# Kernel optimization log

Hardware: AMD Instinct MI355X
Metric: run time of the kernel (lower is better)

## Reference

```python
import jax, jax.numpy as jnp
import numpy as np

SLOPE = 25.0   # snntorch surrogate.fast_sigmoid default slope
THR = 1.0      # snntorch Leaky default threshold
BETA = 0.95
SPIKE_STEPS = 4
NUM_HEADS = 16

@jax.custom_vjp
def spike(u):
    # Heaviside forward, fast-sigmoid surrogate backward
    return (u > 0).astype(u.dtype)

def _spike_fwd(u):
    return spike(u), u

def _spike_bwd(u, g):
    return (g / (SLOPE * jnp.abs(u) + 1.0) ** 2,)

spike.defvjp(_spike_fwd, _spike_bwd)

def lif_mean(cur):
    """Run SPIKE_STEPS of a snntorch Leaky neuron (subtract reset, detached)
    with constant input current `cur`; return mean spike train over time."""
    def step(mem, _):
        reset = jax.lax.stop_gradient(spike(mem - THR))
        mem = BETA * mem + cur - reset * THR
        return mem, spike(mem - THR)
    _, spk = jax.lax.scan(step, jnp.zeros_like(cur), None, length=SPIKE_STEPS)
    return spk.mean(axis=0)

def setup_inputs() -> dict:
    B, S, D = 2, 2048, 1024
    key = jax.random.key(0)
    ks = jax.random.split(key, 9)
    std = 1.0 / np.sqrt(D)
    mkw = lambda k: jax.random.uniform(k, (D, D), jnp.float32, -std, std)
    mkb = lambda k: jax.random.uniform(k, (D,), jnp.float32, -std, std)
    return {
        "x": jax.random.normal(ks[0], (B, S, D), jnp.float32),
        "q_w": mkw(ks[1]), "q_b": mkb(ks[2]),
        "k_w": mkw(ks[3]), "k_b": mkb(ks[4]),
        "v_w": mkw(ks[5]), "v_b": mkb(ks[6]),
        "o_w": mkw(ks[7]), "o_b": mkb(ks[8]),
    }

def reference(x, q_w, q_b, k_w, k_b, v_w, v_b, o_w, o_b):
    B, S, D = x.shape
    H = NUM_HEADS
    Hd = D // H
    # projections -> [B, H, S, Hd]  (weights stored [in, out])
    proj = lambda w, b: (x @ w + b).reshape(B, S, H, Hd).transpose(0, 2, 1, 3)
    q, k, v = proj(q_w, q_b), proj(k_w, k_b), proj(v_w, v_b)
    # LIF spiking recurrence, aggregated over time
    q_agg, k_agg, v_agg = lif_mean(q), lif_mean(k), lif_mean(v)
    # standard scaled dot-product attention on aggregated spikes
    scores = jnp.einsum('bhqd,bhkd->bhqk', q_agg, k_agg) / jnp.sqrt(jnp.float32(Hd))
    attn = jax.nn.softmax(scores, axis=-1)
    out = jnp.einsum('bhqk,bhkd->bhqd', attn, v_agg)
    out = out.transpose(0, 2, 1, 3).reshape(B, S, D)
    return out @ o_w + o_b
```

## Files before the change

kernel.cpp:

```cpp
#include <hip/hip_runtime.h>
#include <hip/hip_bf16.h>
#include <stdint.h>

typedef unsigned short u16;
typedef unsigned int u32;
typedef __bf16 bf16x8 __attribute__((ext_vector_type(8)));
typedef float f32x4 __attribute__((ext_vector_type(4)));
typedef float f32x16 __attribute__((ext_vector_type(16)));
typedef u32 u32x4 __attribute__((ext_vector_type(4)));

#define B_   2
#define S_   2048
#define D_   1024
#define H_   16
#define HD_  64

__device__ __forceinline__ u16 f2bf(float f) {
    u32 u = __float_as_uint(f);
    u32 r = (u + 0x7FFFu + ((u >> 16) & 1u)) >> 16;
    return (u16)r;
}
__device__ __forceinline__ float bf2f(u16 s) { return __uint_as_float(((u32)s) << 16); }

__device__ __forceinline__ f32x4 mfma16(bf16x8 a, bf16x8 b, f32x4 c) {
    return __builtin_amdgcn_mfma_f32_16x16x32_bf16(a, b, c, 0, 0, 0);
}
__device__ __forceinline__ f32x16 mfma32(bf16x8 a, bf16x8 b, f32x16 c) {
    return __builtin_amdgcn_mfma_f32_32x32x16_bf16(a, b, c, 0, 0, 0);
}

__device__ __forceinline__ void gl16(const u16* g, u16* l) {
    __builtin_amdgcn_global_load_lds(
        (const __attribute__((address_space(1))) void*)g,
        (__attribute__((address_space(3))) void*)l, 16, 0, 0);
}

__global__ void prep_kernel(const float* __restrict__ x,
                            const float* __restrict__ qw, const float* __restrict__ kw,
                            const float* __restrict__ vw, const float* __restrict__ ow,
                            u16* __restrict__ xbf, u16* __restrict__ wt_all) {
    __shared__ float tile[32][33];
    const int bid = blockIdx.x;
    const int t = threadIdx.x;
    if (bid < 4096) {
        int i = bid * 256 + t;
        float4 v = reinterpret_cast<const float4*>(x)[i];
        uint2 hp;
        hp.x = (u32)f2bf(v.x) | ((u32)f2bf(v.y) << 16);
        hp.y = (u32)f2bf(v.z) | ((u32)f2bf(v.w) << 16);
        reinterpret_cast<uint2*>(xbf)[i] = hp;
        return;
    }
    const int f = bid - 4096;
    const int z = f >> 10;
    const int bi = (f & 1023) >> 5;
    const int bj = f & 31;
    const float* w = (z == 0) ? qw : (z == 1) ? kw : (z == 2) ? vw : ow;
    u16* thi = wt_all + (size_t)z * 1048576;
    const int tx = t & 31, ty = t >> 5;
#pragma unroll
    for (int k = 0; k < 4; k++) {
        int r = ty + k * 8;
        tile[r][tx] = w[(size_t)(bi * 32 + r) * D_ + bj * 32 + tx];
    }
    __syncthreads();
#pragma unroll
    for (int k = 0; k < 4; k++) {
        int r = ty + k * 8;
        thi[(size_t)(bj * 32 + r) * D_ + bi * 32 + tx] = f2bf(tile[tx][r]);
    }
}

__global__ __launch_bounds__(256, 3)
void qkv_gemm(const u16* __restrict__ Ag, const u16* __restrict__ Bg,
              const float* __restrict__ qb, const float* __restrict__ kb,
              const float* __restrict__ vb,
              u16* __restrict__ o0, u16* __restrict__ o1, u16* __restrict__ o2) {
    __shared__ __align__(16) u16 lA[3][128 * 32];
    __shared__ __align__(16) u16 lB[3][128 * 32];

    const int t = threadIdx.x;
    const int flat = blockIdx.y * 24 + blockIdx.x;
    const int swz = (flat & 7) * 96 + (flat >> 3);
    const int m0 = (swz / 24) * 128;
    const int n0 = (swz % 24) * 128;
    const int wid = t >> 6, lane = t & 63;
    const int wm = wid >> 1, wn = wid & 1;
    const int lr = lane & 15, lg = lane >> 4;

    f32x4 acc[4][4] = {};

    auto STAGE = [&](int buf, int kk) {
        const int k0 = kk * 32;
#pragma unroll
        for (int p = 0; p < 2; p++) {
            int idx = p * 256 + wid * 64 + lane;
            int row = idx >> 2, sl = idx & 3;
            int slx = sl ^ ((row >> 1) & 3);
            gl16(Ag + (size_t)(m0 + row) * D_ + k0 + slx * 8,
                 &lA[buf][(p * 256 + wid * 64) * 8]);
            gl16(Bg + (size_t)(n0 + row) * D_ + k0 + slx * 8,
                 &lB[buf][(p * 256 + wid * 64) * 8]);
        }
    };

    STAGE(0, 0);
    STAGE(1, 1);

    for (int kk = 0; kk < 32; ++kk) {
        if (kk < 31) asm volatile("s_waitcnt vmcnt(4)" ::: "memory");
        else         asm volatile("s_waitcnt vmcnt(0)" ::: "memory");
        __builtin_amdgcn_s_barrier();
        if (kk < 30) STAGE((kk + 2) % 3, kk + 2);

        const int cur = kk % 3;
        bf16x8 af[4], bf[4];
#pragma unroll
        for (int m = 0; m < 4; m++) {
            int row = wm * 64 + m * 16 + lr;
            af[m] = *reinterpret_cast<const bf16x8*>(
                &lA[cur][row * 32 + (lg ^ ((row >> 1) & 3)) * 8]);
        }
#pragma unroll
        for (int n = 0; n < 4; n++) {
            int row = wn * 64 + n * 16 + lr;
            bf[n] = *reinterpret_cast<const bf16x8*>(
                &lB[cur][row * 32 + (lg ^ ((row >> 1) & 3)) * 8]);
        }
#pragma unroll
        for (int m = 0; m < 4; m++)
#pragma unroll
            for (int n = 0; n < 4; n++)
                acc[m][n] = mfma16(af[m], bf[n], acc[m][n]);
    }

    const int col0f = n0 + wn * 64;
    const int proj = col0f >> 10;
    const float* bp = (proj == 0) ? qb : (proj == 1) ? kb : vb;
    u16* dst = (proj == 0) ? o0 : (proj == 1) ? o1 : o2;
#pragma unroll
    for (int m = 0; m < 4; m++) {
#pragma unroll
        for (int n = 0; n < 4; n++) {
            u16 agg4[4];
#pragma unroll
            for (int r = 0; r < 4; r++) {
                int row = m0 + wm * 64 + m * 16 + lg * 4 + r;
                int colp = (col0f + n * 16 + lr) & 1023;
                float cur_i = acc[m][n][r] + bp[colp];
                float mem = 0.f;
                int cnt = 0;
#pragma unroll
                for (int tt = 0; tt < 4; tt++) {
                    float reset = (mem > 1.f) ? 1.f : 0.f;
                    mem = 0.95f * mem;
                    mem = mem + cur_i;
                    mem = mem - reset;
                    cnt += (mem > 1.f) ? 1 : 0;
                }
                u16 agg = (u16)(__float_as_uint((float)cnt * 0.25f) >> 16);
                if (proj != 2) {
                    int b = row >> 11, s = row & 2047;
                    int h = colp >> 6, d = colp & 63;
                    dst[((size_t)(b * H_ + h) * S_ + s) * HD_ + d] = agg;
                } else {
                    agg4[r] = agg;
                }
            }
            if (proj == 2) {
                int row0 = m0 + wm * 64 + m * 16 + lg * 4;
                int colp = (col0f + n * 16 + lr) & 1023;
                int b = row0 >> 11, s = row0 & 2047;
                int h = colp >> 6, d = colp & 63;
                uint2 pk;
                pk.x = (u32)agg4[0] | ((u32)agg4[1] << 16);
                pk.y = (u32)agg4[2] | ((u32)agg4[3] << 16);
                *reinterpret_cast<uint2*>(
                    &dst[((size_t)(b * H_ + h) * HD_ + d) * S_ + s]) = pk;
            }
        }
    }
}

__global__ __launch_bounds__(256, 4)
void o_gemm(const u16* __restrict__ Ag, const u16* __restrict__ Bhg,
            const float* __restrict__ bias, float* __restrict__ out) {
    __shared__ __align__(16) u16 lA[3][64 * 32];
    __shared__ __align__(16) u16 lB[3][64 * 32];

    const int t = threadIdx.x;
    const int flat = blockIdx.y * 16 + blockIdx.x;
    const int swz = (flat & 7) * 128 + (flat >> 3);
    const int m0 = (swz >> 4) * 64;
    const int n0 = (swz & 15) * 64;
    const int wid = t >> 6, lane = t & 63;
    const int wm = wid >> 1, wn = wid & 1;
    const int lr = lane & 15, lg = lane >> 4;

    f32x4 acc[2][2] = {};

    auto STAGE = [&](int buf, int kk) {
        const int k0 = kk * 32;
        int idx = wid * 64 + lane;
        int row = idx >> 2, sl = idx & 3;
        int slx = sl ^ ((row >> 1) & 3);
        gl16(Ag + (size_t)(m0 + row) * D_ + k0 + slx * 8,
             &lA[buf][(wid * 64) * 8]);
        gl16(Bhg + (size_t)(n0 + row) * D_ + k0 + slx * 8,
             &lB[buf][(wid * 64) * 8]);
    };

    STAGE(0, 0);
    STAGE(1, 1);

    for (int kk = 0; kk < 32; ++kk) {
        if (kk < 31) asm volatile("s_waitcnt vmcnt(2)" ::: "memory");
        else         asm volatile("s_waitcnt vmcnt(0)" ::: "memory");
        __builtin_amdgcn_s_barrier();
        if (kk < 30) STAGE((kk + 2) % 3, kk + 2);

        const int cur = kk % 3;
        bf16x8 af[2], bf[2];
#pragma unroll
        for (int m = 0; m < 2; m++) {
            int row = wm * 32 + m * 16 + lr;
            af[m] = *reinterpret_cast<const bf16x8*>(
                &lA[cur][row * 32 + (lg ^ ((row >> 1) & 3)) * 8]);
        }
#pragma unroll
        for (int n = 0; n < 2; n++) {
            int row = wn * 32 + n * 16 + lr;
            bf[n] = *reinterpret_cast<const bf16x8*>(
                &lB[cur][row * 32 + (lg ^ ((row >> 1) & 3)) * 8]);
        }
#pragma unroll
        for (int m = 0; m < 2; m++)
#pragma unroll
            for (int n = 0; n < 2; n++)
                acc[m][n] = mfma16(af[m], bf[n], acc[m][n]);
    }

#pragma unroll
    for (int m = 0; m < 2; m++)
#pragma unroll
        for (int n = 0; n < 2; n++)
#pragma unroll
            for (int r = 0; r < 4; r++) {
                int row = m0 + wm * 32 + m * 16 + lg * 4 + r;
                int col = n0 + wn * 32 + n * 16 + lr;
                out[(size_t)row * D_ + col] = acc[m][n][r] + bias[col];
            }
}

__global__ __launch_bounds__(512, 1)
void attn_kernel(const u16* __restrict__ qa, const u16* __restrict__ ka,
                 const u16* __restrict__ vt, u16* __restrict__ oag) {
    __shared__ __align__(16) u16 Kb[3][2][64 * 64];
    __shared__ __align__(16) u16 Vb[3][2][64 * 64];

    const int t = threadIdx.x;
    const int wid = t >> 6, lane = t & 63;
    const int l31 = lane & 31, hi = lane >> 5;
    const int sx = l31 & 7;

    const int flat = blockIdx.y * 8 + blockIdx.x;
    const int swz = (flat & 7) * 32 + (flat >> 3);
    const int bh = swz >> 3;
    const int q0 = (swz & 7) * 256;

    const u16* qbase = qa + (size_t)bh * S_ * HD_;
    const u16* kbase = ka + (size_t)bh * S_ * HD_;
    const u16* vbase = vt + (size_t)bh * HD_ * S_;

    bf16x8 qf[4];
#pragma unroll
    for (int kc = 0; kc < 4; kc++)
        qf[kc] = *reinterpret_cast<const bf16x8*>(
            qbase + (size_t)(q0 + wid * 32 + l31) * HD_ + kc * 16 + hi * 8);

    bf16x8 ones;
#pragma unroll
    for (int j = 0; j < 8; j++) ones[j] = (__bf16)1.0f;

    f32x16 oacc0 = {}, oacc1 = {}, ssum = {};

    auto STAGE = [&](int buf, int kt2) {
        const int row = t >> 3, sl = t & 7;
        const int slx = sl ^ (row & 7);
        const int lbase = (wid * 64) * 8;
#pragma unroll
        for (int s = 0; s < 2; s++) {
            gl16(kbase + (size_t)((kt2 + s) * 64 + row) * HD_ + slx * 8,
                 &Kb[buf][s][lbase]);
            gl16(vbase + (size_t)row * S_ + (kt2 + s) * 64 + slx * 8,
                 &Vb[buf][s][lbase]);
        }
    };

    auto COMPUTE = [&](const u16* Kt, const u16* Vt) {
        f32x16 sacc[2] = {};
        __builtin_amdgcn_s_setprio(1);
#pragma unroll
        for (int kc = 0; kc < 4; kc++) {
            int sl = (2 * kc + hi) ^ sx;
            bf16x8 k0 = *reinterpret_cast<const bf16x8*>(&Kt[l31 * 64 + sl * 8]);
            bf16x8 k1 = *reinterpret_cast<const bf16x8*>(&Kt[(32 + l31) * 64 + sl * 8]);
            sacc[0] = mfma32(k0, qf[kc], sacc[0]);
            sacc[1] = mfma32(k1, qf[kc], sacc[1]);
        }
        __builtin_amdgcn_s_setprio(0);
        bf16x8 pa[4];
#pragma unroll
        for (int bb = 0; bb < 2; bb++) {
#pragma unroll
            for (int half = 0; half < 2; half++) {
                float pv[8];
#pragma unroll
                for (int r = 0; r < 8; r++) {
                    float tt = __builtin_fmaf(sacc[bb][half * 8 + r],
                                              0.18033688f, -5.7707802f);
                    asm("v_exp_f32 %0, %1" : "=v"(pv[r]) : "v"(tt));
                }
                u32 A1, A2, B1, B2;
                asm("v_cvt_pk_bf16_f32 %0, %1, %2"
                    : "=v"(A1) : "v"(pv[0]), "v"(pv[1]));
                asm("v_cvt_pk_bf16_f32 %0, %1, %2"
                    : "=v"(A2) : "v"(pv[2]), "v"(pv[3]));
                asm("v_cvt_pk_bf16_f32 %0, %1, %2"
                    : "=v"(B1) : "v"(pv[4]), "v"(pv[5]));
                asm("v_cvt_pk_bf16_f32 %0, %1, %2"
                    : "=v"(B2) : "v"(pv[6]), "v"(pv[7]));
                asm("v_permlane32_swap_b32 %0, %1" : "+v"(A1), "+v"(B1));
                asm("v_permlane32_swap_b32 %0, %1" : "+v"(A2), "+v"(B2));
                u32x4 pw;
                pw.x = A1; pw.y = A2; pw.z = B1; pw.w = B2;
                pa[bb * 2 + half] = __builtin_bit_cast(bf16x8, pw);
            }
        }
        __builtin_amdgcn_s_setprio(1);
#pragma unroll
        for (int k4 = 0; k4 < 4; k4++)
            ssum = mfma32(pa[k4], ones, ssum);
#pragma unroll
        for (int k4 = 0; k4 < 4; k4++) {
            int sl = (2 * k4 + hi) ^ sx;
            bf16x8 v0 = *reinterpret_cast<const bf16x8*>(&Vt[l31 * 64 + sl * 8]);
            bf16x8 v1 = *reinterpret_cast<const bf16x8*>(&Vt[(32 + l31) * 64 + sl * 8]);
            oacc0 = mfma32(pa[k4], v0, oacc0);
            oacc1 = mfma32(pa[k4], v1, oacc1);
        }
        __builtin_amdgcn_s_setprio(0);
    };

    STAGE(0, 0);
    STAGE(1, 2);

    for (int pt = 0; pt < 16; ++pt) {
        if (pt < 15) asm volatile("s_waitcnt vmcnt(4)" ::: "memory");
        else         asm volatile("s_waitcnt vmcnt(0)" ::: "memory");
        __builtin_amdgcn_s_barrier();
        if (pt < 14) STAGE((pt + 2) % 3, (pt + 2) * 2);

        const int cur = pt % 3;
        COMPUTE(&Kb[cur][0][0], &Vb[cur][0][0]);
        COMPUTE(&Kb[cur][1][0], &Vb[cur][1][0]);
    }

    const int b = bh >> 4, h = bh & 15;
#pragma unroll
    for (int r = 0; r < 16; r++) {
        int q = q0 + wid * 32 + (r & 3) + 8 * (r >> 2) + 4 * hi;
        size_t base = (size_t)(b * S_ + q) * D_ + h * 64;
        float v0 = oacc0[r] / ssum[r];
        float v1 = oacc1[r] / ssum[r];
        oag[base + l31] = f2bf(v0);
        oag[base + 32 + l31] = f2bf(v1);
    }
}

extern "C" void kernel_launch(void* const* d_in, const int* in_sizes, int n_in,
                              void* d_out, int out_size, void* d_ws, size_t ws_size,
                              hipStream_t stream) {
    (void)in_sizes; (void)n_in; (void)out_size; (void)ws_size;
    const float* x  = (const float*)d_in[0];
    const float* qw = (const float*)d_in[1];
    const float* qb = (const float*)d_in[2];
    const float* kw = (const float*)d_in[3];
    const float* kb = (const float*)d_in[4];
    const float* vw = (const float*)d_in[5];
    const float* vb = (const float*)d_in[6];
    const float* ow = (const float*)d_in[7];
    const float* ob = (const float*)d_in[8];

    u16* ws = (u16*)d_ws;
    const size_t C = 4194304;
    u16* xbf = ws + 0 * C;
    u16* wt  = ws + 1 * C;
    u16* qag = ws + 2 * C;
    u16* kag = ws + 3 * C;
    u16* vtg = ws + 4 * C;
    u16* oag = ws + 5 * C;

    prep_kernel<<<8192, 256, 0, stream>>>(x, qw, kw, vw, ow, xbf, wt);

    qkv_gemm<<<dim3(24, 32), 256, 0, stream>>>(
        xbf, wt, qb, kb, vb, qag, kag, vtg);
    attn_kernel<<<dim3(8, 32), 512, 0, stream>>>(qag, kag, vtg, oag);
    o_gemm<<<dim3(16, 64), 256, 0, stream>>>(
        oag, wt + 3 * 1048576, ob, (float*)d_out);
}
```

Baseline: 107.1 us.

## Software-pipeline attention so next QK^T MFMA overlaps previous softmax

Splits the per-tile attention compute into QK^T, softmax and PV stages. The loop is reordered so the QK^T for the second half-tile is issued early and its softmax and PV run in the next iteration, interleaved with the next tile's QK^T. The goal is to hide the exp and convert work behind MFMA work. The LDS ring grows from 3 to 4 buffers because the previous tile's V must stay resident, which raises shared memory use and keeps extra score accumulators live in registers.

```diff
diff --git a/kernel.cpp b/kernel.cpp
--- a/kernel.cpp
+++ b/kernel.cpp
@@ -255,8 +255,8 @@
 __global__ __launch_bounds__(512, 1)
 void attn_kernel(const u16* __restrict__ qa, const u16* __restrict__ ka,
                  const u16* __restrict__ vt, u16* __restrict__ oag) {
-    __shared__ __align__(16) u16 Kb[3][2][64 * 64];
-    __shared__ __align__(16) u16 Vb[3][2][64 * 64];
+    __shared__ __align__(16) u16 Kb[4][2][64 * 64];
+    __shared__ __align__(16) u16 Vb[4][2][64 * 64];
 
     const int t = threadIdx.x;
     const int wid = t >> 6, lane = t & 63;
@@ -283,6 +283,7 @@
     for (int j = 0; j < 8; j++) ones[j] = (__bf16)1.0f;
 
     f32x16 oacc0 = {}, oacc1 = {}, ssum = {};
+    f32x16 shold[2];
 
     auto STAGE = [&](int buf, int kt2) {
         const int row = t >> 3, sl = t & 7;
@@ -297,8 +298,7 @@
         }
     };
 
-    auto COMPUTE = [&](const u16* Kt, const u16* Vt) {
-        f32x16 sacc[2] = {};
+    auto QKT = [&](const u16* Kt, f32x16* sacc) {
         __builtin_amdgcn_s_setprio(1);
 #pragma unroll
         for (int kc = 0; kc < 4; kc++) {
@@ -309,7 +309,9 @@
             sacc[1] = mfma32(k1, qf[kc], sacc[1]);
         }
         __builtin_amdgcn_s_setprio(0);
-        bf16x8 pa[4];
+    };
+
+    auto SOFTMAX = [&](const f32x16* sacc, bf16x8* pa) {
 #pragma unroll
         for (int bb = 0; bb < 2; bb++) {
 #pragma unroll
@@ -337,6 +339,9 @@
                 pa[bb * 2 + half] = __builtin_bit_cast(bf16x8, pw);
             }
         }
+    };
+
+    auto PV = [&](const u16* Vt, const bf16x8* pa) {
         __builtin_amdgcn_s_setprio(1);
 #pragma unroll
         for (int k4 = 0; k4 < 4; k4++)
@@ -355,15 +360,43 @@
     STAGE(0, 0);
     STAGE(1, 2);
 
-    for (int pt = 0; pt < 16; ++pt) {
+    asm volatile("s_waitcnt vmcnt(4)" ::: "memory");
+    __builtin_amdgcn_s_barrier();
+    STAGE(2, 4);
+    {
+        f32x16 s0[2] = {};
+        QKT(&Kb[0][0][0], s0);
+        bf16x8 pa0[4];
+        SOFTMAX(s0, pa0);
+        PV(&Vb[0][0][0], pa0);
+        shold[0] = (f32x16){}; shold[1] = (f32x16){};
+        QKT(&Kb[0][1][0], shold);
+    }
+
+    for (int pt = 1; pt < 16; ++pt) {
         if (pt < 15) asm volatile("s_waitcnt vmcnt(4)" ::: "memory");
         else         asm volatile("s_waitcnt vmcnt(0)" ::: "memory");
         __builtin_amdgcn_s_barrier();
-        if (pt < 14) STAGE((pt + 2) % 3, (pt + 2) * 2);
-
-        const int cur = pt % 3;
-        COMPUTE(&Kb[cur][0][0], &Vb[cur][0][0]);
-        COMPUTE(&Kb[cur][1][0], &Vb[cur][1][0]);
+        if (pt < 14) STAGE((pt + 2) & 3, (pt + 2) * 2);
+
+        const int cur = pt & 3, prev = (pt - 1) & 3;
+
+        f32x16 s0[2] = {};
+        QKT(&Kb[cur][0][0], s0);
+        bf16x8 pah[4];
+        SOFTMAX(shold, pah);
+        PV(&Vb[prev][1][0], pah);
+        bf16x8 pa0[4];
+        SOFTMAX(s0, pa0);
+        PV(&Vb[cur][0][0], pa0);
+        shold[0] = (f32x16){}; shold[1] = (f32x16){};
+        QKT(&Kb[cur][1][0], shold);
+    }
+
+    {
+        bf16x8 pah[4];
+        SOFTMAX(shold, pah);
+        PV(&Vb[15 & 3][1][0], pah);
     }
 
     const int b = bh >> 4, h = bh & 15;
```

New measurement: 112.6 us. 1.05x slower.
